# Performance work log

Hardware: AMD Instinct MI355X
Metric: run time of the kernel (lower is better)

## Reference

```python
import jax, jax.numpy as jnp
import numpy as np

D_MODEL = 256
D_FFN = 1024
N_HEADS = 8
N_LEVELS = 4
N_POINTS = 4
SPATIAL = np.array([[60, 100], [30, 50], [15, 25], [8, 13]], dtype=np.int32)  # (H, W) per level


def _layer_norm(x, g, b, eps=1e-5):
    mu = jnp.mean(x, axis=-1, keepdims=True)
    var = jnp.mean(jnp.square(x - mu), axis=-1, keepdims=True)
    return (x - mu) * jax.lax.rsqrt(var + eps) * g + b


def _bilinear_sample(v_l, loc, aw, H, W):
    # v_l: (B,H,W,h,hd); loc: (B,Lq,h,p,2) normalized [0,1]; aw: (B,Lq,h,p)
    B = v_l.shape[0]
    h = v_l.shape[3]
    x = loc[..., 0] * W - 0.5  # grid_sample align_corners=False convention
    y = loc[..., 1] * H - 0.5
    x0 = jnp.floor(x)
    y0 = jnp.floor(y)
    lx = x - x0
    ly = y - y0
    x0i = x0.astype(jnp.int32)
    y0i = y0.astype(jnp.int32)
    bi = jnp.arange(B)[:, None, None, None]
    hi = jnp.arange(h)[None, None, :, None]

    def g(xi, yi):
        valid = (xi >= 0) & (xi < W) & (yi >= 0) & (yi < H)
        xc = jnp.clip(xi, 0, W - 1)
        yc = jnp.clip(yi, 0, H - 1)
        return v_l[bi, yc, xc, hi] * valid[..., None].astype(v_l.dtype)  # zero padding

    w00 = (1 - lx) * (1 - ly)
    w01 = lx * (1 - ly)
    w10 = (1 - lx) * ly
    w11 = lx * ly
    samp = (g(x0i, y0i) * w00[..., None] + g(x0i + 1, y0i) * w01[..., None]
            + g(x0i, y0i + 1) * w10[..., None] + g(x0i + 1, y0i + 1) * w11[..., None])
    # weighted sum over sampling points -> (B,Lq,h,hd)
    return jnp.einsum('blhpd,blhp->blhd', samp, aw)


def _msda(q, val, ref, W_value, b_value, W_off, b_off, W_attn, b_attn, W_out, b_out):
    # mmcv MultiScaleDeformableAttention (batch_first, identity=query, eval-mode dropout)
    B, Lq, C = q.shape
    hd = C // N_HEADS
    v = (val @ W_value + b_value).reshape(B, -1, N_HEADS, hd)
    off = (q @ W_off + b_off).reshape(B, Lq, N_HEADS, N_LEVELS, N_POINTS, 2)
    aw = jax.nn.softmax((q @ W_attn + b_attn).reshape(B, Lq, N_HEADS, N_LEVELS * N_POINTS), axis=-1)
    aw = aw.reshape(B, Lq, N_HEADS, N_LEVELS, N_POINTS)
    normalizer = jnp.asarray(SPATIAL[:, ::-1].copy(), dtype=q.dtype)  # (levels, 2) = (W, H)
    loc = ref[:, :, None, :, None, :] + off / normalizer[None, None, None, :, None, :]
    out = jnp.zeros((B, Lq, N_HEADS, hd), q.dtype)
    start = 0
    for lvl in range(N_LEVELS):
        H, W = int(SPATIAL[lvl, 0]), int(SPATIAL[lvl, 1])
        v_l = v[:, start:start + H * W].reshape(B, H, W, N_HEADS, hd)
        start += H * W
        out = out + _bilinear_sample(v_l, loc[:, :, :, lvl], aw[:, :, :, lvl], H, W)
    return q + out.reshape(B, Lq, C) @ W_out + b_out  # identity + output_proj


def setup_inputs() -> dict:
    key = jax.random.key(0)
    ks = jax.random.split(key, 16)
    bs, cams, nq = 1, 6, 6400
    l = int(SPATIAL.prod(axis=1).sum())
    s = 0.02
    inp = {
        'query': jax.random.normal(ks[0], (bs, nq, D_MODEL), jnp.float32),
        'key': jax.random.normal(ks[1], (bs, cams, l, D_MODEL), jnp.float32),
        'value': jax.random.normal(ks[2], (bs, cams, l, D_MODEL), jnp.float32),
        'reference_points_cam': jax.random.uniform(ks[3], (cams, bs, nq, N_LEVELS, 2), jnp.float32),
        'spatial_shapes': jnp.asarray(SPATIAL),
        'level_start_index': jnp.asarray(np.concatenate([[0], np.cumsum(SPATIAL.prod(axis=1))[:-1]]).astype(np.int32)),
        'bev_mask': jax.random.randint(ks[4], (cams, bs, nq, 4), 0, 2).astype(jnp.int32),
        'W_value': jax.random.normal(ks[5], (D_MODEL, D_MODEL), jnp.float32) * s,
        'b_value': jnp.zeros((D_MODEL,), jnp.float32),
        'W_off': jax.random.normal(ks[6], (D_MODEL, N_HEADS * N_LEVELS * N_POINTS * 2), jnp.float32) * s,
        'b_off': jax.random.normal(ks[7], (N_HEADS * N_LEVELS * N_POINTS * 2,), jnp.float32) * s,
        'W_attn': jax.random.normal(ks[8], (D_MODEL, N_HEADS * N_LEVELS * N_POINTS), jnp.float32) * s,
        'b_attn': jnp.zeros((N_HEADS * N_LEVELS * N_POINTS,), jnp.float32),
        'W_out': jax.random.normal(ks[9], (D_MODEL, D_MODEL), jnp.float32) * s,
        'b_out': jnp.zeros((D_MODEL,), jnp.float32),
        'ln1_g': jnp.ones((D_MODEL,), jnp.float32),
        'ln1_b': jnp.zeros((D_MODEL,), jnp.float32),
        'W1': jax.random.normal(ks[10], (D_MODEL, D_FFN), jnp.float32) * s,
        'b1': jnp.zeros((D_FFN,), jnp.float32),
        'W2': jax.random.normal(ks[11], (D_FFN, D_MODEL), jnp.float32) * s,
        'b2': jnp.zeros((D_MODEL,), jnp.float32),
        'ln2_g': jnp.ones((D_MODEL,), jnp.float32),
        'ln2_b': jnp.zeros((D_MODEL,), jnp.float32),
    }
    return inp


def reference(query, key, value, reference_points_cam, spatial_shapes, level_start_index, bev_mask,
              W_value, b_value, W_off, b_off, W_attn, b_attn, W_out, b_out,
              ln1_g, ln1_b, W1, b1, W2, b2, ln2_g, ln2_b):
    bs, nq, C = query.shape
    cams = key.shape[1]
    l = key.shape[2]
    # per-camera query visibility taken from batch element 0 (as in original)
    cam_mask = (bev_mask[:, 0].sum(-1) > 0).astype(query.dtype)  # (cams, nq)
    # rebatch via masking: equivalent to gather-to-padded since attention is per-query
    q_rb = (query[:, None] * cam_mask[None, :, :, None]).reshape(bs * cams, nq, C)
    ref_rb = (jnp.transpose(reference_points_cam, (1, 0, 2, 3, 4))
              * cam_mask[None, :, :, None, None]).reshape(bs * cams, nq, N_LEVELS, 2)
    val = value.reshape(bs * cams, l, C)
    attn = _msda(q_rb, val, ref_rb, W_value, b_value, W_off, b_off, W_attn, b_attn, W_out, b_out)
    attn = attn.reshape(bs, cams, nq, C)
    # scatter-add back (only visible camera contributions)
    slots = jnp.einsum('bknc,kn->bnc', attn, cam_mask)
    # visibility count (full bev_mask, per batch element)
    count = (bev_mask.sum(-1) > 0).astype(query.dtype)  # (cams, bs, nq)
    count = jnp.maximum(count.transpose(1, 2, 0).sum(-1), 1.0)  # (bs, nq)
    slots = slots / count[..., None]
    x = _layer_norm(slots + query, ln1_g, ln1_b)
    ffn = jax.nn.relu(x @ W1 + b1) @ W2 + b2
    return _layer_norm(x + ffn, ln2_g, ln2_b)
```

## Files before the change

### kernel.cpp

```cpp
#include <hip/hip_runtime.h>
#include <math.h>

#define NQ      6400
#define NCAMS   6
#define LTOT    7979
#define DM      256
#define DFFN    1024

typedef __attribute__((ext_vector_type(8))) short bf16x8;
typedef __attribute__((ext_vector_type(4))) float f32x4;
typedef __attribute__((ext_vector_type(2))) float f32x2;

__device__ inline unsigned short f32_to_bf16(float f) {
    unsigned u = __float_as_uint(f);
    unsigned r = u + 0x7FFF + ((u >> 16) & 1);
    return (unsigned short)(r >> 16);
}

__device__ inline unsigned cvt_pk_bf16(float lo, float hi) {
    unsigned r;
    asm("v_cvt_pk_bf16_f32 %0, %1, %2" : "=v"(r) : "v"(lo), "v"(hi));
    return r;
}

__global__ __launch_bounds__(256) void wt_head_kernel(
    const float* __restrict__ Wv, const float* __restrict__ Woff,
    const float* __restrict__ Wattn, unsigned short* __restrict__ wsT)
{
    int b = blockIdx.x;
    const float* src; int K, N, t0, dstoff;
    if (b < 64)       { src = Wv;    K = 256; N = 256; t0 = 0;   dstoff = 0; }
    else if (b < 128) { src = Woff;  K = 256; N = 256; t0 = 64;  dstoff = 65536; }
    else              { src = Wattn; K = 256; N = 128; t0 = 128; dstoff = 131072; }
    int t = b - t0;
    int ntn = N >> 5;
    int kt = t / ntn, nt = t - kt * ntn;
    __shared__ float tile[32][33];
    int tx = threadIdx.x & 31, ty = threadIdx.x >> 5;
    #pragma unroll
    for (int i = 0; i < 4; ++i)
        tile[ty + i * 8][tx] = src[(size_t)(kt * 32 + ty + i * 8) * N + nt * 32 + tx];
    __syncthreads();
    #pragma unroll
    for (int i = 0; i < 4; ++i) {
        int nn = nt * 32 + ty + i * 8;
        wsT[dstoff + (size_t)nn * K + kt * 32 + tx] = f32_to_bf16(tile[tx][ty + i * 8]);
    }
}

__global__ __launch_bounds__(256) void head_kernel(
    const float* __restrict__ value, const float* __restrict__ query,
    const unsigned short* __restrict__ WvT, const unsigned short* __restrict__ WqT,
    const float* __restrict__ bv, const float* __restrict__ boff,
    const float* __restrict__ battn,
    unsigned char* __restrict__ vb, unsigned short* __restrict__ qoffb,
    unsigned short* __restrict__ qawb)
{
    __shared__ __align__(16) unsigned char smem[20480];
    const int b = blockIdx.x;
    const int tid = threadIdx.x;
    const int wave = tid >> 6, lane = tid & 63;
    const int wm = wave >> 1, wn = wave & 1;
    const int quad = lane >> 4, l16 = lane & 15;

    if (b < 750) {
        unsigned short (*As)[40] = (unsigned short(*)[40])smem;
        unsigned short (*Bs)[40] = (unsigned short(*)[40])(smem + 10240);
        const int m0 = (b >> 1) * 128, n0 = (b & 1) * 128;
        const int M = NCAMS * LTOT;

        f32x4 acc[4][4] = {};

        for (int k0 = 0; k0 < 256; k0 += 32) {
            #pragma unroll
            for (int i = 0; i < 2; ++i) {
                int idx = tid + 256 * i;
                int r = idx >> 2, kc = (idx & 3) * 8;
                int gr = m0 + r;
                float4 f0, f1;
                if (gr < M) {
                    f0 = *(const float4*)(value + (size_t)gr * 256 + k0 + kc);
                    f1 = *(const float4*)(value + (size_t)gr * 256 + k0 + kc + 4);
                } else { f0 = make_float4(0.f,0.f,0.f,0.f); f1 = f0; }
                uint4 o;
                o.x = cvt_pk_bf16(f0.x, f0.y);
                o.y = cvt_pk_bf16(f0.z, f0.w);
                o.z = cvt_pk_bf16(f1.x, f1.y);
                o.w = cvt_pk_bf16(f1.z, f1.w);
                *(uint4*)&As[r][kc] = o;
            }
            #pragma unroll
            for (int i = 0; i < 2; ++i) {
                int idx = tid + 256 * i;
                int r = idx >> 2, kc = (idx & 3) * 8;
                *(uint4*)&Bs[r][kc] = *(const uint4*)(WvT + (size_t)(n0 + r) * 256 + k0 + kc);
            }
            __syncthreads();
            bf16x8 af[4], bfr[4];
            #pragma unroll
            for (int mi = 0; mi < 4; ++mi)
                af[mi] = *(const bf16x8*)&As[wm * 64 + mi * 16 + l16][quad * 8];
            #pragma unroll
            for (int ni = 0; ni < 4; ++ni)
                bfr[ni] = *(const bf16x8*)&Bs[wn * 64 + ni * 16 + l16][quad * 8];
            #pragma unroll
            for (int mi = 0; mi < 4; ++mi)
                #pragma unroll
                for (int ni = 0; ni < 4; ++ni)
                    acc[mi][ni] = __builtin_amdgcn_mfma_f32_16x16x32_bf16(
                        af[mi], bfr[ni], acc[mi][ni], 0, 0, 0);
            __syncthreads();
        }

        #pragma unroll
        for (int mi = 0; mi < 4; ++mi) {
            #pragma unroll
            for (int r = 0; r < 4; ++r) {
                int gm = m0 + wm * 64 + mi * 16 + quad * 4 + r;
                if (gm >= M) continue;
                int cam = gm / LTOT;
                int pix = gm - cam * LTOT;
                #pragma unroll
                for (int p = 0; p < 2; ++p) {
                    int gn0 = n0 + wn * 64 + p * 32 + l16;
                    int head = gn0 >> 5;
                    float v0 = acc[mi][2 * p][r]     + bv[gn0];
                    float v1 = acc[mi][2 * p + 1][r] + bv[gn0 + 16];
                    int pk = __builtin_amdgcn_cvt_pk_fp8_f32(v0, v1, 0, false);
                    *(unsigned short*)(vb + (((size_t)(cam * 8 + head)) * LTOT + pix) * 32
                                       + 2 * l16) = (unsigned short)pk;
                }
            }
        }
    } else {
        unsigned short (*As)[40] = (unsigned short(*)[40])smem;
        unsigned short (*Bs)[40] = (unsigned short(*)[40])(smem + 5120);
        const int t = b - 750;
        const int bx = t / 100, by = t % 100;
        const int m0 = by * 64, n0 = bx * 128;
        const int is_attn = (bx == 2);

        f32x4 acc[2][4] = {};

        for (int k0 = 0; k0 < 256; k0 += 32) {
            {
                int r = tid >> 2, kc = (tid & 3) * 8;
                float4 f0 = *(const float4*)(query + (size_t)(m0 + r) * 256 + k0 + kc);
                float4 f1 = *(const float4*)(query + (size_t)(m0 + r) * 256 + k0 + kc + 4);
                uint4 o;
                o.x = cvt_pk_bf16(f0.x, f0.y);
                o.y = cvt_pk_bf16(f0.z, f0.w);
                o.z = cvt_pk_bf16(f1.x, f1.y);
                o.w = cvt_pk_bf16(f1.z, f1.w);
                *(uint4*)&As[r][kc] = o;
            }
            #pragma unroll
            for (int i = 0; i < 2; ++i) {
                int idx = tid + 256 * i;
                int r = idx >> 2, kc = (idx & 3) * 8;
                *(uint4*)&Bs[r][kc] = *(const uint4*)(WqT + (size_t)(n0 + r) * 256 + k0 + kc);
            }
            __syncthreads();
            bf16x8 af[2], bfr[4];
            #pragma unroll
            for (int mi = 0; mi < 2; ++mi)
                af[mi] = *(const bf16x8*)&As[wm * 32 + mi * 16 + l16][quad * 8];
            #pragma unroll
            for (int ni = 0; ni < 4; ++ni)
                bfr[ni] = *(const bf16x8*)&Bs[wn * 64 + ni * 16 + l16][quad * 8];
            #pragma unroll
            for (int mi = 0; mi < 2; ++mi)
                #pragma unroll
                for (int ni = 0; ni < 4; ++ni)
                    acc[mi][ni] = __builtin_amdgcn_mfma_f32_16x16x32_bf16(
                        af[mi], bfr[ni], acc[mi][ni], 0, 0, 0);
            __syncthreads();
        }

        if (is_attn) {
            #pragma unroll
            for (int mi = 0; mi < 2; ++mi) {
                #pragma unroll
                for (int r = 0; r < 4; ++r) {
                    int gm = m0 + wm * 32 + mi * 16 + quad * 4 + r;
                    #pragma unroll
                    for (int ni = 0; ni < 4; ++ni) {
                        int gn = wn * 64 + ni * 16 + l16;
                        float v = acc[mi][ni][r] + battn[gn];
                        float mx = v;
                        #pragma unroll
                        for (int s = 1; s < 16; s <<= 1)
                            mx = fmaxf(mx, __shfl_xor(mx, s, 64));
                        float e = __expf(v - mx);
                        float sum = e;
                        #pragma unroll
                        for (int s = 1; s < 16; s <<= 1)
                            sum += __shfl_xor(sum, s, 64);
                        qawb[(size_t)gm * 128 + gn] = f32_to_bf16(e / sum);
                    }
                }
            }
        } else {
            #pragma unroll
            for (int mi = 0; mi < 2; ++mi) {
                #pragma unroll
                for (int r = 0; r < 4; ++r) {
                    int gm = m0 + wm * 32 + mi * 16 + quad * 4 + r;
                    #pragma unroll
                    for (int ni = 0; ni < 4; ++ni) {
                        int gn = n0 + wn * 64 + ni * 16 + l16;
                        qoffb[(size_t)gm * 256 + gn] = f32_to_bf16(acc[mi][ni][r] + boff[gn]);
                    }
                }
            }
        }
    }
}

__global__ __launch_bounds__(256) void sample_kernel(
    const unsigned char* __restrict__ vb,
    const unsigned short* __restrict__ qoffb,
    const unsigned short* __restrict__ qawb,
    const float* __restrict__ refpts,
    const int*   __restrict__ bev_mask,
    const float* __restrict__ Wout, const float* __restrict__ W1,
    const float* __restrict__ W2,
    unsigned short* __restrict__ outsum,
    float* __restrict__ visb,
    unsigned short* __restrict__ wsT)
{
    __shared__ __align__(16) unsigned s_tab[NCAMS][272][4];
    __shared__ float s_vis[NCAMS][16];
    __shared__ int   s_nvis[16];

    const int bid = blockIdx.x;
    const int tid = threadIdx.x;

    if (bid >= 3200) {
        int t = bid - 3200;
        const float* src; int K, N, dstoff;
        if (t < 64)       { src = Wout; K = 256;  N = 256;  dstoff = 163840; }
        else if (t < 320) { src = W1;   K = 256;  N = 1024; dstoff = 229376; t -= 64; }
        else              { src = W2;   K = 1024; N = 256;  dstoff = 491520; t -= 320; }
        int ntn = N >> 5;
        int kt = t / ntn, nt = t - kt * ntn;
        float (*tile)[33] = (float(*)[33])&s_tab[0][0][0];
        int tx = tid & 31, ty = tid >> 5;
        #pragma unroll
        for (int i = 0; i < 4; ++i)
            tile[ty + i * 8][tx] = src[(size_t)(kt * 32 + ty + i * 8) * N + nt * 32 + tx];
        __syncthreads();
        int txp = (dstoff == 163840) ? (((tx & 15) << 1) | (tx >> 4)) : tx;
        #pragma unroll
        for (int i = 0; i < 4; ++i) {
            int nn = nt * 32 + ty + i * 8;
            wsT[dstoff + (size_t)nn * K + kt * 32 + txp] = f32_to_bf16(tile[tx][ty + i * 8]);
        }
        return;
    }

    const int h   = bid & 7;
    const int q0  = (bid >> 3) * 16;
    const int sq  = tid >> 4;
    const int tup = tid & 15;
    const int lvl = tup >> 2;
    const int n_s = q0 + sq;

    if (tid < 96) {
        int cam = tid >> 4, q = tid & 15;
        const int* bm = bev_mask + ((size_t)cam * NQ + q0 + q) * 4;
        s_vis[cam][q] = ((bm[0] + bm[1] + bm[2] + bm[3]) > 0) ? 1.f : 0.f;
    }
    __syncthreads();
    if (tid >= 32 && tid < 48) {
        int q = tid - 32;
        float s = 0.f;
        #pragma unroll
        for (int cam = 0; cam < NCAMS; ++cam) s += s_vis[cam][q];
        s_nvis[q] = (int)s;
    }

    unsigned uoff = *(const unsigned*)(qoffb + (size_t)n_s * 256 + h * 32 + tup * 2);
    const float offx  = __uint_as_float(uoff << 16);
    const float offy  = __uint_as_float(uoff & 0xFFFF0000u);
    const float my_aw = __uint_as_float((unsigned)qawb[(size_t)n_s * 128 + h * 16 + tup] << 16);
    const int Wl   = (lvl == 0) ? 100 : (lvl == 1) ? 50 : (lvl == 2) ? 25 : 13;
    const int Hl   = (lvl == 0) ? 60  : (lvl == 1) ? 30 : (lvl == 2) ? 15 : 8;
    const int base = (lvl == 0) ? 0   : (lvl == 1) ? 6000 : (lvl == 2) ? 7500 : 7875;
    const float dx = offx / (float)Wl;
    const float dy = offy / (float)Hl;
    const int tabi = sq * 17 + tup;

    float2 rp[NCAMS];
    #pragma unroll
    for (int k = 0; k < NCAMS; ++k)
        rp[k] = *(const float2*)(refpts + (((size_t)k * NQ + n_s) * 4 + lvl) * 2);
    __syncthreads();

    #pragma unroll
    for (int k = 0; k < NCAMS; ++k) {
        float fx = (rp[k].x + dx) * (float)Wl - 0.5f;
        float fy = (rp[k].y + dy) * (float)Hl - 0.5f;
        float x0f = floorf(fx), y0f = floorf(fy);
        float lx = fx - x0f, ly = fy - y0f;
        int x0 = (int)x0f, y0 = (int)y0f;
        int x1 = x0 + 1, y1 = y0 + 1;
        float wb = my_aw * s_vis[k][sq];
        float w00 = (1.f - lx) * (1.f - ly) * wb;
        float w01 = lx * (1.f - ly) * wb;
        float w10 = (1.f - lx) * ly * wb;
        float w11 = lx * ly * wb;
        bool vx0 = (x0 >= 0) & (x0 < Wl), vx1 = (x1 >= 0) & (x1 < Wl);
        bool vy0 = (y0 >= 0) & (y0 < Hl), vy1 = (y1 >= 0) & (y1 < Hl);
        uint4 o;
        o.x = (vx0 & vy0) ? (((unsigned)(base + y0 * Wl + x0) << 16) | f32_to_bf16(w00)) : 0u;
        o.y = (vx1 & vy0) ? (((unsigned)(base + y0 * Wl + x1) << 16) | f32_to_bf16(w01)) : 0u;
        o.z = (vx0 & vy1) ? (((unsigned)(base + y1 * Wl + x0) << 16) | f32_to_bf16(w10)) : 0u;
        o.w = (vx1 & vy1) ? (((unsigned)(base + y1 * Wl + x1) << 16) | f32_to_bf16(w11)) : 0u;
        *(uint4*)&s_tab[k][tabi][0] = o;
    }
    __syncthreads();

    const int tp  = (tid >> 1) & 7;
    const int cg2 = tid & 1;

    f32x2 A[8] = {};

    #pragma unroll
    for (int k = 0; k < NCAMS; ++k) {
        const char* vkh = (const char*)vb + (size_t)(k * 8 + h) * (LTOT * 32) + cg2 * 16;
        #pragma unroll
        for (int t = 0; t < 2; ++t) {
            uint4 t4 = *(const uint4*)&s_tab[k][sq * 17 + tp * 2 + t][0];
            #pragma unroll
            for (int corner = 0; corner < 4; ++corner) {
                unsigned tc = (corner == 0) ? t4.x : (corner == 1) ? t4.y
                            : (corner == 2) ? t4.z : t4.w;
                float w = __uint_as_float(tc << 16);
                f32x2 w2 = {w, w};
                uint4 d = *(const uint4*)(vkh + ((size_t)(tc >> 16) << 5));
                A[0] += w2 * __builtin_amdgcn_cvt_pk_f32_fp8(d.x, false);
                A[1] += w2 * __builtin_amdgcn_cvt_pk_f32_fp8(d.x, true);
                A[2] += w2 * __builtin_amdgcn_cvt_pk_f32_fp8(d.y, false);
                A[3] += w2 * __builtin_amdgcn_cvt_pk_f32_fp8(d.y, true);
                A[4] += w2 * __builtin_amdgcn_cvt_pk_f32_fp8(d.z, false);
                A[5] += w2 * __builtin_amdgcn_cvt_pk_f32_fp8(d.z, true);
                A[6] += w2 * __builtin_amdgcn_cvt_pk_f32_fp8(d.w, false);
                A[7] += w2 * __builtin_amdgcn_cvt_pk_f32_fp8(d.w, true);
            }
        }
    }

    #pragma unroll
    for (int i = 0; i < 8; ++i) {
        float x0 = A[i].x, x1 = A[i].y;
        x0 += __shfl_xor(x0, 2, 64); x1 += __shfl_xor(x1, 2, 64);
        x0 += __shfl_xor(x0, 4, 64); x1 += __shfl_xor(x1, 4, 64);
        x0 += __shfl_xor(x0, 8, 64); x1 += __shfl_xor(x1, 8, 64);
        A[i].x = x0; A[i].y = x1;
    }

    if ((tid & 14) == 0) {
        int nv = s_nvis[sq];
        float sc = 1.f / (float)(nv > 0 ? nv : 1);
        uint4 o0, o1;
        o0.x = f32_to_bf16(A[0].x * sc) | ((unsigned)f32_to_bf16(A[0].y * sc) << 16);
        o0.y = f32_to_bf16(A[1].x * sc) | ((unsigned)f32_to_bf16(A[1].y * sc) << 16);
        o0.z = f32_to_bf16(A[2].x * sc) | ((unsigned)f32_to_bf16(A[2].y * sc) << 16);
        o0.w = f32_to_bf16(A[3].x * sc) | ((unsigned)f32_to_bf16(A[3].y * sc) << 16);
        o1.x = f32_to_bf16(A[4].x * sc) | ((unsigned)f32_to_bf16(A[4].y * sc) << 16);
        o1.y = f32_to_bf16(A[5].x * sc) | ((unsigned)f32_to_bf16(A[5].y * sc) << 16);
        o1.z = f32_to_bf16(A[6].x * sc) | ((unsigned)f32_to_bf16(A[6].y * sc) << 16);
        o1.w = f32_to_bf16(A[7].x * sc) | ((unsigned)f32_to_bf16(A[7].y * sc) << 16);
        *(uint4*)(outsum + (size_t)n_s * 256 + h * 32 + cg2 * 16)     = o0;
        *(uint4*)(outsum + (size_t)n_s * 256 + h * 32 + cg2 * 16 + 8) = o1;
    }
    if (h == 0 && tid < 16) visb[q0 + tid] = (s_nvis[tid] > 0) ? 1.f : 0.f;
}

__global__ __launch_bounds__(256) void projln1_kernel(
    const unsigned short* __restrict__ A, const unsigned short* __restrict__ BT,
    const float* __restrict__ query, const float* __restrict__ visb,
    const float* __restrict__ b_out, const float* __restrict__ g,
    const float* __restrict__ b,
    float* __restrict__ xout, unsigned short* __restrict__ xb16)
{
    const int K = 256;
    __shared__ __align__(16) unsigned short As[32][40];
    __shared__ __align__(16) unsigned short Bs[256][40];
    __shared__ float sred[2][4][4][2];
    __shared__ float ssred[2][4][4][2];
    __shared__ float s_mu[32], s_rs[32];

    const int tid  = threadIdx.x;
    const int wave = tid >> 6, lane = tid & 63;
    const int wm = wave >> 1, wn = wave & 1;
    const int quad = lane >> 4, l16 = lane & 15;
    const int m0 = blockIdx.x * 32;

    f32x4 acc[8] = {};

    for (int k0 = 0; k0 < K; k0 += 32) {
        {
            int r = tid >> 3, kc = (tid & 7) * 4;
            *(uint2*)&As[r][kc] = *(const uint2*)(A + (size_t)(m0 + r) * K + k0 + kc);
        }
        {
            const unsigned short* src = BT + (size_t)tid * K + k0;
            *(uint4*)&Bs[tid][0]  = *(const uint4*)(src);
            *(uint4*)&Bs[tid][8]  = *(const uint4*)(src + 8);
            *(uint4*)&Bs[tid][16] = *(const uint4*)(src + 16);
            *(uint4*)&Bs[tid][24] = *(const uint4*)(src + 24);
        }
        __syncthreads();
        bf16x8 af = *(const bf16x8*)&As[wm * 16 + l16][quad * 8];
        #pragma unroll
        for (int ni = 0; ni < 8; ++ni) {
            bf16x8 bfr = *(const bf16x8*)&Bs[wn * 128 + ni * 16 + l16][quad * 8];
            acc[ni] = __builtin_amdgcn_mfma_f32_16x16x32_bf16(af, bfr, acc[ni], 0, 0, 0);
        }
        __syncthreads();
    }

    float vals[8][4];
    #pragma unroll
    for (int r = 0; r < 4; ++r) {
        int gm = m0 + wm * 16 + quad * 4 + r;
        float vs = visb[gm];
        float s = 0.f, ss = 0.f;
        #pragma unroll
        for (int ni = 0; ni < 8; ++ni) {
            int gn = wn * 128 + ni * 16 + l16;
            float v = acc[ni][r] + vs * b_out[gn]
                    + query[(size_t)gm * 256 + gn] * (1.f + vs);
            vals[ni][r] = v;
            s += v; ss += v * v;
        }
        #pragma unroll
        for (int m = 1; m < 16; m <<= 1) {
            s  += __shfl_xor(s,  m, 64);
            ss += __shfl_xor(ss, m, 64);
        }
        if (l16 == 0) {
            sred[wm][quad][r][wn]  = s;
            ssred[wm][quad][r][wn] = ss;
        }
    }
    __syncthreads();
    if (tid < 32) {
        int lwm = tid >> 4, lq = (tid >> 2) & 3, lr = tid & 3;
        float s  = sred[lwm][lq][lr][0]  + sred[lwm][lq][lr][1];
        float ss = ssred[lwm][lq][lr][0] + ssred[lwm][lq][lr][1];
        float mu = s * (1.f / 256.f);
        float var = ss * (1.f / 256.f) - mu * mu;
        s_mu[tid] = mu;
        s_rs[tid] = rsqrtf(var + 1e-5f);
    }
    __syncthreads();

    #pragma unroll
    for (int r = 0; r < 4; ++r) {
        int rowl = wm * 16 + quad * 4 + r;
        int gm = m0 + rowl;
        float mu = s_mu[rowl], rs = s_rs[rowl];
        #pragma unroll
        for (int ni = 0; ni < 8; ++ni) {
            int gn = wn * 128 + ni * 16 + l16;
            float res = (vals[ni][r] - mu) * rs * g[gn] + b[gn];
            xout[(size_t)gm * 256 + gn] = res;
            xb16[(size_t)gm * 256 + gn] = f32_to_bf16(res);
        }
    }
}

__global__ __launch_bounds__(256) void gemm64_kernel(
    const unsigned short* __restrict__ A, const unsigned short* __restrict__ BT,
    const float* __restrict__ bias, unsigned short* __restrict__ Cb,
    int M, int N, int K, int mode)
{
    __shared__ __align__(16) unsigned short As[64][40];
    __shared__ __align__(16) unsigned short Bs[128][40];

    const int tid  = threadIdx.x;
    const int wave = tid >> 6, lane = tid & 63;
    const int wm = wave >> 1, wn = wave & 1;
    const int quad = lane >> 4, l16 = lane & 15;
    const int m0 = blockIdx.y * 64, n0 = blockIdx.x * 128;
    const int nz = gridDim.z;
    const int klen = K / nz;
    const int kbase = blockIdx.z * klen;

    f32x4 acc[2][4] = {};

    for (int k0 = kbase; k0 < kbase + klen; k0 += 32) {
        {
            int r = tid >> 2, kc = (tid & 3) * 8;
            int gr = m0 + r;
            uint4 d = (gr < M) ? *(const uint4*)(A + (size_t)gr * K + k0 + kc)
                               : make_uint4(0u, 0u, 0u, 0u);
            *(uint4*)&As[r][kc] = d;
        }
        #pragma unroll
        for (int i = 0; i < 2; ++i) {
            int idx = tid + 256 * i;
            int r = idx >> 2, kc = (idx & 3) * 8;
            *(uint4*)&Bs[r][kc] = *(const uint4*)(BT + (size_t)(n0 + r) * K + k0 + kc);
        }
        __syncthreads();
        bf16x8 af[2], bfr[4];
        #pragma unroll
        for (int mi = 0; mi < 2; ++mi)
            af[mi] = *(const bf16x8*)&As[wm * 32 + mi * 16 + l16][quad * 8];
        #pragma unroll
        for (int ni = 0; ni < 4; ++ni)
            bfr[ni] = *(const bf16x8*)&Bs[wn * 64 + ni * 16 + l16][quad * 8];
        #pragma unroll
        for (int mi = 0; mi < 2; ++mi)
            #pragma unroll
            for (int ni = 0; ni < 4; ++ni)
                acc[mi][ni] = __builtin_amdgcn_mfma_f32_16x16x32_bf16(
                    af[mi], bfr[ni], acc[mi][ni], 0, 0, 0);
        __syncthreads();
    }

    const float* bz = (blockIdx.z == 0) ? bias : nullptr;
    unsigned short* Cz = Cb + (size_t)blockIdx.z * M * N;

    #pragma unroll
    for (int mi = 0; mi < 2; ++mi) {
        #pragma unroll
        for (int r = 0; r < 4; ++r) {
            int gm = m0 + wm * 32 + mi * 16 + quad * 4 + r;
            if (gm >= M) continue;
            #pragma unroll
            for (int ni = 0; ni < 4; ++ni) {
                int gn = n0 + wn * 64 + ni * 16 + l16;
                float v = acc[mi][ni][r] + (bz ? bz[gn] : 0.f);
                if (mode == 1) v = fmaxf(v, 0.f);
                Cz[(size_t)gm * N + gn] = f32_to_bf16(v);
            }
        }
    }
}

__global__ __launch_bounds__(256) void ln2v_kernel(
    const float* __restrict__ x, const unsigned short* __restrict__ f0,
    const unsigned short* __restrict__ f1,
    const float* __restrict__ g, const float* __restrict__ b,
    float* __restrict__ out)
{
    int row  = blockIdx.x * 4 + (threadIdx.x >> 6);
    int lane = threadIdx.x & 63;
    size_t base = (size_t)row * 256 + lane * 4;
    float4 xv = *(const float4*)(x + base);
    uint2 u0 = *(const uint2*)(f0 + base);
    uint2 u1 = *(const uint2*)(f1 + base);
    float t0 = xv.x + __uint_as_float(u0.x << 16)        + __uint_as_float(u1.x << 16);
    float t1 = xv.y + __uint_as_float(u0.x & 0xFFFF0000u) + __uint_as_float(u1.x & 0xFFFF0000u);
    float t2 = xv.z + __uint_as_float(u0.y << 16)        + __uint_as_float(u1.y << 16);
    float t3 = xv.w + __uint_as_float(u0.y & 0xFFFF0000u) + __uint_as_float(u1.y & 0xFFFF0000u);
    float s  = t0 + t1 + t2 + t3;
    float ss = t0 * t0 + t1 * t1 + t2 * t2 + t3 * t3;
    #pragma unroll
    for (int m = 1; m < 64; m <<= 1) {
        s  += __shfl_xor(s,  m, 64);
        ss += __shfl_xor(ss, m, 64);
    }
    float mu = s * (1.f / 256.f);
    float rs = rsqrtf(ss * (1.f / 256.f) - mu * mu + 1e-5f);
    float4 gv = *(const float4*)(g + lane * 4);
    float4 bv = *(const float4*)(b + lane * 4);
    float4 o;
    o.x = (t0 - mu) * rs * gv.x + bv.x;
    o.y = (t1 - mu) * rs * gv.y + bv.y;
    o.z = (t2 - mu) * rs * gv.z + bv.z;
    o.w = (t3 - mu) * rs * gv.w + bv.w;
    *(float4*)(out + base) = o;
}

extern "C" void kernel_launch(void* const* d_in, const int* in_sizes, int n_in,
                              void* d_out, int out_size, void* d_ws, size_t ws_size,
                              hipStream_t stream)
{
    const float* query   = (const float*)d_in[0];
    const float* value   = (const float*)d_in[2];
    const float* refpts  = (const float*)d_in[3];
    const int*   bevmask = (const int*)d_in[6];
    const float* W_value = (const float*)d_in[7];
    const float* b_value = (const float*)d_in[8];
    const float* W_off   = (const float*)d_in[9];
    const float* b_off   = (const float*)d_in[10];
    const float* W_attn  = (const float*)d_in[11];
    const float* b_attn  = (const float*)d_in[12];
    const float* W_out   = (const float*)d_in[13];
    const float* b_out   = (const float*)d_in[14];
    const float* ln1_g   = (const float*)d_in[15];
    const float* ln1_b   = (const float*)d_in[16];
    const float* W1      = (const float*)d_in[17];
    const float* b1      = (const float*)d_in[18];
    const float* W2      = (const float*)d_in[19];
    const float* b2      = (const float*)d_in[20];
    const float* ln2_g   = (const float*)d_in[21];
    const float* ln2_b   = (const float*)d_in[22];
    float* out = (float*)d_out;

    char* ws = (char*)d_ws;
    unsigned char*  vb     = (unsigned char*)(ws + 0);
    float*          xbuf   = (float*)(ws + 0);
    unsigned short* hbf    = (unsigned short*)(ws + 13000000);
    unsigned short* qoffb  = (unsigned short*)(ws + 27000000);
    unsigned short* xb16   = (unsigned short*)(ws + 27000000);
    unsigned short* qawb   = (unsigned short*)(ws + 31000000);
    unsigned short* outsum = (unsigned short*)(ws + 33000000);
    float*          visb   = (float*)(ws + 36500000);
    unsigned short* wsT    = (unsigned short*)(ws + 36600000);
    unsigned short* ffnout = (unsigned short*)(ws + 39000000);

    unsigned short* WvT = wsT;
    unsigned short* WqT = wsT + 65536;
    unsigned short* WoT = wsT + 163840;
    unsigned short* W1T = wsT + 229376;
    unsigned short* W2T = wsT + 491520;

    wt_head_kernel<<<dim3(160), 256, 0, stream>>>(
        W_value, W_off, W_attn, wsT);
    head_kernel<<<dim3(1050), 256, 0, stream>>>(
        value, query, WvT, WqT, b_value, b_off, b_attn, vb, qoffb, qawb);
    sample_kernel<<<dim3(3776), 256, 0, stream>>>(
        vb, qoffb, qawb, refpts, bevmask, W_out, W1, W2, outsum, visb, wsT);
    projln1_kernel<<<dim3(200), 256, 0, stream>>>(
        outsum, WoT, query, visb, b_out, ln1_g, ln1_b, xbuf, xb16);
    gemm64_kernel<<<dim3(8, 100, 1), 256, 0, stream>>>(
        xb16, W1T, b1, hbf, NQ, DFFN, 256, 1);
    gemm64_kernel<<<dim3(2, 100, 2), 256, 0, stream>>>(
        hbf, W2T, b2, ffnout, NQ, 256, DFFN, 2);
    ln2v_kernel<<<dim3(1600), 256, 0, stream>>>(
        xbuf, ffnout, ffnout + (size_t)NQ * 256, ln2_g, ln2_b, out);
}
```

Baseline: 279.5 us.

## Fuse output projection, LN1, FFN and LN2 into one tail kernel

Replaces the projln1, two FFN GEMM, and ln2 kernels with a single kernel in which each block of 32 rows keeps the LN1 output and FFN hidden chunks in shared memory. This removes the global round-trips for x, the 1024-wide hidden activation and the split-K partials, plus three launches. The cost is that only 200 blocks run the whole FFN, with every block re-streaming W1 and W2 from global memory, so parallelism drops and the kernel may be latency- or bandwidth-bound on weight loads.

```diff
diff --git a/kernel.cpp b/kernel.cpp
--- a/kernel.cpp
+++ b/kernel.cpp
@@ -21,6 +21,9 @@
     unsigned r;
     asm("v_cvt_pk_bf16_f32 %0, %1, %2" : "=v"(r) : "v"(lo), "v"(hi));
     return r;
+}
+__device__ inline unsigned short cvt1_bf16(float x) {
+    return (unsigned short)cvt_pk_bf16(x, 0.f);
 }
 
 __global__ __launch_bounds__(256) void wt_head_kernel(
@@ -378,16 +381,23 @@
     if (h == 0 && tid < 16) visb[q0 + tid] = (s_nvis[tid] > 0) ? 1.f : 0.f;
 }
 
-__global__ __launch_bounds__(256) void projln1_kernel(
-    const unsigned short* __restrict__ A, const unsigned short* __restrict__ BT,
+__global__ __launch_bounds__(256) void tail_kernel(
+    const unsigned short* __restrict__ A,
+    const unsigned short* __restrict__ BT,
+    const unsigned short* __restrict__ W1T,
+    const unsigned short* __restrict__ W2T,
     const float* __restrict__ query, const float* __restrict__ visb,
-    const float* __restrict__ b_out, const float* __restrict__ g,
-    const float* __restrict__ b,
-    float* __restrict__ xout, unsigned short* __restrict__ xb16)
+    const float* __restrict__ b_out,
+    const float* __restrict__ g1, const float* __restrict__ bln1,
+    const float* __restrict__ fb1, const float* __restrict__ fb2,
+    const float* __restrict__ g2, const float* __restrict__ bln2,
+    float* __restrict__ out)
 {
-    const int K = 256;
     __shared__ __align__(16) unsigned short As[32][40];
     __shared__ __align__(16) unsigned short Bs[256][40];
+    __shared__ __align__(16) unsigned short Bs2[128][72];
+    __shared__ __align__(16) unsigned short xs[32][264];
+    __shared__ __align__(16) unsigned short hs[32][136];
     __shared__ float sred[2][4][4][2];
     __shared__ float ssred[2][4][4][2];
     __shared__ float s_mu[32], s_rs[32];
@@ -400,13 +410,13 @@
 
     f32x4 acc[8] = {};
 
-    for (int k0 = 0; k0 < K; k0 += 32) {
+    for (int k0 = 0; k0 < 256; k0 += 32) {
         {
             int r = tid >> 3, kc = (tid & 7) * 4;
-            *(uint2*)&As[r][kc] = *(const uint2*)(A + (size_t)(m0 + r) * K + k0 + kc);
+            *(uint2*)&As[r][kc] = *(const uint2*)(A + (size_t)(m0 + r) * 256 + k0 + kc);
         }
         {
-            const unsigned short* src = BT + (size_t)tid * K + k0;
+            const unsigned short* src = BT + (size_t)tid * 256 + k0;
             *(uint4*)&Bs[tid][0]  = *(const uint4*)(src);
             *(uint4*)&Bs[tid][8]  = *(const uint4*)(src + 8);
             *(uint4*)&Bs[tid][16] = *(const uint4*)(src + 16);
@@ -461,121 +471,113 @@
     #pragma unroll
     for (int r = 0; r < 4; ++r) {
         int rowl = wm * 16 + quad * 4 + r;
+        float mu = s_mu[rowl], rs = s_rs[rowl];
+        #pragma unroll
+        for (int ni = 0; ni < 8; ++ni) {
+            int gn = wn * 128 + ni * 16 + l16;
+            float res = (vals[ni][r] - mu) * rs * g1[gn] + bln1[gn];
+            vals[ni][r] = res;
+            xs[rowl][gn] = cvt1_bf16(res);
+        }
+    }
+
+    f32x4 acc2[8] = {};
+
+    for (int nc = 0; nc < 8; ++nc) {
+        f32x4 hacc[4] = {};
+        for (int k0 = 0; k0 < 256; k0 += 64) {
+            #pragma unroll
+            for (int i = 0; i < 4; ++i) {
+                int idx = tid + 256 * i;
+                int rr = idx >> 3, c8 = (idx & 7) * 8;
+                *(uint4*)&Bs2[rr][c8] =
+                    *(const uint4*)(W1T + (size_t)(nc * 128 + rr) * 256 + k0 + c8);
+            }
+            __syncthreads();
+            #pragma unroll
+            for (int s = 0; s < 2; ++s) {
+                bf16x8 a2 = *(const bf16x8*)&xs[wm * 16 + l16][k0 + s * 32 + quad * 8];
+                #pragma unroll
+                for (int ni = 0; ni < 4; ++ni) {
+                    bf16x8 b2v = *(const bf16x8*)&Bs2[wn * 64 + ni * 16 + l16][s * 32 + quad * 8];
+                    hacc[ni] = __builtin_amdgcn_mfma_f32_16x16x32_bf16(a2, b2v, hacc[ni], 0, 0, 0);
+                }
+            }
+            __syncthreads();
+        }
+        #pragma unroll
+        for (int ni = 0; ni < 4; ++ni) {
+            #pragma unroll
+            for (int r = 0; r < 4; ++r) {
+                int rowl = wm * 16 + quad * 4 + r;
+                int col  = wn * 64 + ni * 16 + l16;
+                hs[rowl][col] = cvt1_bf16(fmaxf(hacc[ni][r] + fb1[nc * 128 + col], 0.f));
+            }
+        }
+        __syncthreads();
+        #pragma unroll
+        for (int ks = 0; ks < 4; ++ks) {
+            {
+                const unsigned short* src = W2T + (size_t)tid * 1024 + nc * 128 + ks * 32;
+                *(uint4*)&Bs[tid][0]  = *(const uint4*)(src);
+                *(uint4*)&Bs[tid][8]  = *(const uint4*)(src + 8);
+                *(uint4*)&Bs[tid][16] = *(const uint4*)(src + 16);
+                *(uint4*)&Bs[tid][24] = *(const uint4*)(src + 24);
+            }
+            __syncthreads();
+            bf16x8 a3 = *(const bf16x8*)&hs[wm * 16 + l16][ks * 32 + quad * 8];
+            #pragma unroll
+            for (int ni = 0; ni < 8; ++ni) {
+                bf16x8 b3 = *(const bf16x8*)&Bs[wn * 128 + ni * 16 + l16][quad * 8];
+                acc2[ni] = __builtin_amdgcn_mfma_f32_16x16x32_bf16(a3, b3, acc2[ni], 0, 0, 0);
+            }
+            __syncthreads();
+        }
+    }
+
+    #pragma unroll
+    for (int r = 0; r < 4; ++r) {
+        float s = 0.f, ss = 0.f;
+        #pragma unroll
+        for (int ni = 0; ni < 8; ++ni) {
+            int gn = wn * 128 + ni * 16 + l16;
+            float t = vals[ni][r] + acc2[ni][r] + fb2[gn];
+            vals[ni][r] = t;
+            s += t; ss += t * t;
+        }
+        #pragma unroll
+        for (int m = 1; m < 16; m <<= 1) {
+            s  += __shfl_xor(s,  m, 64);
+            ss += __shfl_xor(ss, m, 64);
+        }
+        if (l16 == 0) {
+            sred[wm][quad][r][wn]  = s;
+            ssred[wm][quad][r][wn] = ss;
+        }
+    }
+    __syncthreads();
+    if (tid < 32) {
+        int lwm = tid >> 4, lq = (tid >> 2) & 3, lr = tid & 3;
+        float s  = sred[lwm][lq][lr][0]  + sred[lwm][lq][lr][1];
+        float ss = ssred[lwm][lq][lr][0] + ssred[lwm][lq][lr][1];
+        float mu = s * (1.f / 256.f);
+        float var = ss * (1.f / 256.f) - mu * mu;
+        s_mu[tid] = mu;
+        s_rs[tid] = rsqrtf(var + 1e-5f);
+    }
+    __syncthreads();
+
+    #pragma unroll
+    for (int r = 0; r < 4; ++r) {
+        int rowl = wm * 16 + quad * 4 + r;
         int gm = m0 + rowl;
         float mu = s_mu[rowl], rs = s_rs[rowl];
         #pragma unroll
         for (int ni = 0; ni < 8; ++ni) {
             int gn = wn * 128 + ni * 16 + l16;
-            float res = (vals[ni][r] - mu) * rs * g[gn] + b[gn];
-            xout[(size_t)gm * 256 + gn] = res;
-            xb16[(size_t)gm * 256 + gn] = f32_to_bf16(res);
-        }
-    }
-}
-
-__global__ __launch_bounds__(256) void gemm64_kernel(
-    const unsigned short* __restrict__ A, const unsigned short* __restrict__ BT,
-    const float* __restrict__ bias, unsigned short* __restrict__ Cb,
-    int M, int N, int K, int mode)
-{
-    __shared__ __align__(16) unsigned short As[64][40];
-    __shared__ __align__(16) unsigned short Bs[128][40];
-
-    const int tid  = threadIdx.x;
-    const int wave = tid >> 6, lane = tid & 63;
-    const int wm = wave >> 1, wn = wave & 1;
-    const int quad = lane >> 4, l16 = lane & 15;
-    const int m0 = blockIdx.y * 64, n0 = blockIdx.x * 128;
-    const int nz = gridDim.z;
-    const int klen = K / nz;
-    const int kbase = blockIdx.z * klen;
-
-    f32x4 acc[2][4] = {};
-
-    for (int k0 = kbase; k0 < kbase + klen; k0 += 32) {
-        {
-            int r = tid >> 2, kc = (tid & 3) * 8;
-            int gr = m0 + r;
-            uint4 d = (gr < M) ? *(const uint4*)(A + (size_t)gr * K + k0 + kc)
-                               : make_uint4(0u, 0u, 0u, 0u);
-            *(uint4*)&As[r][kc] = d;
-        }
-        #pragma unroll
-        for (int i = 0; i < 2; ++i) {
-            int idx = tid + 256 * i;
-            int r = idx >> 2, kc = (idx & 3) * 8;
-            *(uint4*)&Bs[r][kc] = *(const uint4*)(BT + (size_t)(n0 + r) * K + k0 + kc);
-        }
-        __syncthreads();
-        bf16x8 af[2], bfr[4];
-        #pragma unroll
-        for (int mi = 0; mi < 2; ++mi)
-            af[mi] = *(const bf16x8*)&As[wm * 32 + mi * 16 + l16][quad * 8];
-        #pragma unroll
-        for (int ni = 0; ni < 4; ++ni)
-            bfr[ni] = *(const bf16x8*)&Bs[wn * 64 + ni * 16 + l16][quad * 8];
-        #pragma unroll
-        for (int mi = 0; mi < 2; ++mi)
-            #pragma unroll
-            for (int ni = 0; ni < 4; ++ni)
-                acc[mi][ni] = __builtin_amdgcn_mfma_f32_16x16x32_bf16(
-                    af[mi], bfr[ni], acc[mi][ni], 0, 0, 0);
-        __syncthreads();
-    }
-
-    const float* bz = (blockIdx.z == 0) ? bias : nullptr;
-    unsigned short* Cz = Cb + (size_t)blockIdx.z * M * N;
-
-    #pragma unroll
-    for (int mi = 0; mi < 2; ++mi) {
-        #pragma unroll
-        for (int r = 0; r < 4; ++r) {
-            int gm = m0 + wm * 32 + mi * 16 + quad * 4 + r;
-            if (gm >= M) continue;
-            #pragma unroll
-            for (int ni = 0; ni < 4; ++ni) {
-                int gn = n0 + wn * 64 + ni * 16 + l16;
-                float v = acc[mi][ni][r] + (bz ? bz[gn] : 0.f);
-                if (mode == 1) v = fmaxf(v, 0.f);
-                Cz[(size_t)gm * N + gn] = f32_to_bf16(v);
-            }
-        }
-    }
-}
-
-__global__ __launch_bounds__(256) void ln2v_kernel(
-    const float* __restrict__ x, const unsigned short* __restrict__ f0,
-    const unsigned short* __restrict__ f1,
-    const float* __restrict__ g, const float* __restrict__ b,
-    float* __restrict__ out)
-{
-    int row  = blockIdx.x * 4 + (threadIdx.x >> 6);
-    int lane = threadIdx.x & 63;
-    size_t base = (size_t)row * 256 + lane * 4;
-    float4 xv = *(const float4*)(x + base);
-    uint2 u0 = *(const uint2*)(f0 + base);
-    uint2 u1 = *(const uint2*)(f1 + base);
-    float t0 = xv.x + __uint_as_float(u0.x << 16)        + __uint_as_float(u1.x << 16);
-    float t1 = xv.y + __uint_as_float(u0.x & 0xFFFF0000u) + __uint_as_float(u1.x & 0xFFFF0000u);
-    float t2 = xv.z + __uint_as_float(u0.y << 16)        + __uint_as_float(u1.y << 16);
-    float t3 = xv.w + __uint_as_float(u0.y & 0xFFFF0000u) + __uint_as_float(u1.y & 0xFFFF0000u);
-    float s  = t0 + t1 + t2 + t3;
-    float ss = t0 * t0 + t1 * t1 + t2 * t2 + t3 * t3;
-    #pragma unroll
-    for (int m = 1; m < 64; m <<= 1) {
-        s  += __shfl_xor(s,  m, 64);
-        ss += __shfl_xor(ss, m, 64);
-    }
-    float mu = s * (1.f / 256.f);
-    float rs = rsqrtf(ss * (1.f / 256.f) - mu * mu + 1e-5f);
-    float4 gv = *(const float4*)(g + lane * 4);
-    float4 bv = *(const float4*)(b + lane * 4);
-    float4 o;
-    o.x = (t0 - mu) * rs * gv.x + bv.x;
-    o.y = (t1 - mu) * rs * gv.y + bv.y;
-    o.z = (t2 - mu) * rs * gv.z + bv.z;
-    o.w = (t3 - mu) * rs * gv.w + bv.w;
-    *(float4*)(out + base) = o;
+            out[(size_t)gm * 256 + gn] = (vals[ni][r] - mu) * rs * g2[gn] + bln2[gn];
+        }
+    }
 }
 
 extern "C" void kernel_launch(void* const* d_in, const int* in_sizes, int n_in,
@@ -606,15 +608,11 @@
 
     char* ws = (char*)d_ws;
     unsigned char*  vb     = (unsigned char*)(ws + 0);
-    float*          xbuf   = (float*)(ws + 0);
-    unsigned short* hbf    = (unsigned short*)(ws + 13000000);
     unsigned short* qoffb  = (unsigned short*)(ws + 27000000);
-    unsigned short* xb16   = (unsigned short*)(ws + 27000000);
     unsigned short* qawb   = (unsigned short*)(ws + 31000000);
     unsigned short* outsum = (unsigned short*)(ws + 33000000);
     float*          visb   = (float*)(ws + 36500000);
     unsigned short* wsT    = (unsigned short*)(ws + 36600000);
-    unsigned short* ffnout = (unsigned short*)(ws + 39000000);
 
     unsigned short* WvT = wsT;
     unsigned short* WqT = wsT + 65536;
@@ -628,12 +626,7 @@
         value, query, WvT, WqT, b_value, b_off, b_attn, vb, qoffb, qawb);
     sample_kernel<<<dim3(3776), 256, 0, stream>>>(
         vb, qoffb, qawb, refpts, bevmask, W_out, W1, W2, outsum, visb, wsT);
-    projln1_kernel<<<dim3(200), 256, 0, stream>>>(
-        outsum, WoT, query, visb, b_out, ln1_g, ln1_b, xbuf, xb16);
-    gemm64_kernel<<<dim3(8, 100, 1), 256, 0, stream>>>(
-        xb16, W1T, b1, hbf, NQ, DFFN, 256, 1);
-    gemm64_kernel<<<dim3(2, 100, 2), 256, 0, stream>>>(
-        hbf, W2T, b2, ffnout, NQ, 256, DFFN, 2);
-    ln2v_kernel<<<dim3(1600), 256, 0, stream>>>(
-        xbuf, ffnout, ffnout + (size_t)NQ * 256, ln2_g, ln2_b, out);
-}
+    tail_kernel<<<dim3(200), 256, 0, stream>>>(
+        outsum, WoT, W1T, W2T, query, visb, b_out,
+        ln1_g, ln1_b, b1, b2, ln2_g, ln2_b, out);
+}
```

New measurement: 285.3 us. 2.1% more time.
